# Kernel optimization log

Measured on AMD Instinct MI355X. Metric: run time of the kernel, lower is better.

Reference implementation:

```python
import jax, jax.numpy as jnp
import numpy as np

B, N, C = 256, 196, 256
RES, RES_, STRIDE = 14, 7, 2
H, KD, D = 16, 16, 64          # heads, key_dim, d=attn_ratio*key_dim
NH_KD, DH = H * KD, H * D      # 256, 1024
HW = DH + NH_KD                # kv width 1280
OUT = 512
EPS = 1e-5
SCALE = KD ** -0.5


def make_bias_idxs():
    pts = [(i, j) for i in range(RES) for j in range(RES)]
    pts_ = [(i, j) for i in range(RES_) for j in range(RES_)]
    offsets, idxs = {}, []
    for p1 in pts_:
        for p2 in pts:
            off = (abs(p1[0] * STRIDE - p2[0]), abs(p1[1] * STRIDE - p2[1]))
            if off not in offsets:
                offsets[off] = len(offsets)
            idxs.append(offsets[off])
    return np.array(idxs, np.int32).reshape(len(pts_), len(pts)), len(offsets)


def bn(x, g, b, m, v):
    return (x - m) * (g / jnp.sqrt(v + EPS)) + b


def hardswish(x):
    return x * jnp.clip(x + 3.0, 0.0, 6.0) / 6.0


def setup_inputs() -> dict:
    key = jax.random.key(0)
    ks = jax.random.split(key, 12)
    idxs, n_off = make_bias_idxs()
    s_in, s_dh = (2.0 / C) ** 0.5, (2.0 / DH) ** 0.5
    return {
        "x": jax.random.normal(ks[0], (B, N, C), jnp.float32),
        "W_kv": jax.random.normal(ks[1], (HW, C), jnp.float32) * s_in,
        "g_kv": jnp.ones((HW,)), "b_kv": jnp.zeros((HW,)),
        "m_kv": jax.random.normal(ks[2], (HW,)) * 0.1,
        "v_kv": jax.random.uniform(ks[3], (HW,), minval=0.5, maxval=1.5),
        "W_q": jax.random.normal(ks[4], (NH_KD, C), jnp.float32) * s_in,
        "g_q": jnp.ones((NH_KD,)), "b_q": jnp.zeros((NH_KD,)),
        "m_q": jax.random.normal(ks[5], (NH_KD,)) * 0.1,
        "v_q": jax.random.uniform(ks[6], (NH_KD,), minval=0.5, maxval=1.5),
        "W_p": jax.random.normal(ks[7], (OUT, DH), jnp.float32) * s_dh,
        "g_p": jnp.ones((OUT,)), "b_p": jnp.zeros((OUT,)),
        "m_p": jax.random.normal(ks[8], (OUT,)) * 0.1,
        "v_p": jax.random.uniform(ks[9], (OUT,), minval=0.5, maxval=1.5),
        "attn_biases": jax.random.normal(ks[10], (H, n_off), jnp.float32) * 0.02,
        "bias_idxs": jnp.asarray(idxs),
    }


def reference(x, W_kv, g_kv, b_kv, m_kv, v_kv, W_q, g_q, b_q, m_q, v_q,
              W_p, g_p, b_p, m_p, v_p, attn_biases, bias_idxs):
    # kv branch: Linear(no bias) + BN over flattened tokens
    kv = bn(jnp.einsum('bnc,hc->bnh', x, W_kv), g_kv, b_kv, m_kv, v_kv)
    kv = kv.reshape(B, N, H, KD + D)
    k, v = kv[..., :KD], kv[..., KD:]                 # [B,N,H,KD], [B,N,H,D]
    # q branch: spatial subsample stride 2 then LinearNorm
    xs = x.reshape(B, RES, RES, C)[:, ::STRIDE, ::STRIDE].reshape(B, RES_ * RES_, C)
    q = bn(jnp.einsum('bnc,hc->bnh', xs, W_q), g_q, b_q, m_q, v_q)
    q = q.reshape(B, RES_ * RES_, H, KD)              # [B,49,H,KD]
    bias = attn_biases[:, bias_idxs]                  # [H,49,196]
    attn = jnp.einsum('bqhd,bkhd->bhqk', q, k) * SCALE + bias
    attn = jax.nn.softmax(attn, axis=-1)
    o = jnp.einsum('bhqk,bkhd->bqhd', attn, v).reshape(B, RES_ * RES_, DH)
    return bn(jnp.einsum('bnd,od->bno', hardswish(o), W_p), g_p, b_p, m_p, v_p)
```

## Files before the change

kernel.cpp:

```cpp
#include <hip/hip_runtime.h>

typedef unsigned short u16;
typedef unsigned int u32;
typedef __attribute__((ext_vector_type(8))) short bf16x8;
typedef __attribute__((ext_vector_type(4))) float f32x4;

__device__ __forceinline__ u16 f2bf(float x) {
  union { float f; u32 u; } un; un.f = x;
  u32 r = un.u + 0x7FFFu + ((un.u >> 16) & 1u);
  return (u16)(r >> 16);
}

__device__ __forceinline__ void gl_lds16(const u16* gsrc, u16* ldst) {
  __builtin_amdgcn_global_load_lds(
      (const __attribute__((address_space(1))) void*)gsrc,
      (__attribute__((address_space(3))) void*)ldst,
      16, 0, 0);
}

__global__ __launch_bounds__(256) void prep_misc(
    const float* __restrict__ Wkv, const float* __restrict__ Wq, const float* __restrict__ Wp,
    const float* __restrict__ gkv, const float* __restrict__ bkv, const float* __restrict__ mkv, const float* __restrict__ vkv,
    const float* __restrict__ gq, const float* __restrict__ bq, const float* __restrict__ mq, const float* __restrict__ vq,
    const float* __restrict__ gp, const float* __restrict__ bp, const float* __restrict__ mp, const float* __restrict__ vp,
    const float* __restrict__ ab, const int* __restrict__ bidx,
    u16* __restrict__ wkvb, u16* __restrict__ wqb, u16* __restrict__ wpb,
    float* __restrict__ skv, float* __restrict__ tkv,
    float* __restrict__ sq, float* __restrict__ tq,
    float* __restrict__ sp, float* __restrict__ tp,
    float* __restrict__ biasf)
{
  int i = blockIdx.x * 256 + threadIdx.x;
  if (i < 327680) { wkvb[i] = f2bf(Wkv[i]); return; }
  i -= 327680;
  if (i < 65536) { wqb[i] = f2bf(Wq[i]); return; }
  i -= 65536;
  if (i < 524288) { wpb[i] = f2bf(Wp[i]); return; }
  i -= 524288;
  if (i < 153664) { biasf[i] = ab[(i / 9604) * 196 + bidx[i % 9604]]; return; }
  i -= 153664;
  if (i < 1280) { float s = gkv[i] * rsqrtf(vkv[i] + 1e-5f); skv[i] = s; tkv[i] = bkv[i] - mkv[i] * s; return; }
  i -= 1280;
  if (i < 256) {
    int h = i >> 4, c = i & 15;
    float sk = gkv[h * 80 + c] * rsqrtf(vkv[h * 80 + c] + 1e-5f);
    float s = gq[i] * rsqrtf(vq[i] + 1e-5f);
    sq[i] = s * 0.25f * sk;
    tq[i] = (bq[i] - mq[i] * s) * 0.25f * sk;
    return;
  }
  i -= 256;
  if (i < 512) { float s = gp[i] * rsqrtf(vp[i] + 1e-5f); sp[i] = s; tp[i] = bp[i] - mp[i] * s; return; }
}

__global__ __launch_bounds__(256) void conv_x(const float* __restrict__ x, u16* __restrict__ xb)
{
  int u = blockIdx.x * 256 + threadIdx.x;
  float4 v = ((const float4*)x)[u];
  uint2 o;
  o.x = (u32)f2bf(v.x) | ((u32)f2bf(v.y) << 16);
  o.y = (u32)f2bf(v.z) | ((u32)f2bf(v.w) << 16);
  ((uint2*)xb)[u] = o;
}

__global__ __launch_bounds__(256) void gemm_bn(
    const u16* __restrict__ A, const u16* __restrict__ W,
    const float* __restrict__ sv, const float* __restrict__ tv,
    float* __restrict__ outp, int N, int K, int NBLK)
{
  __shared__ u16 As[128 * 64];
  __shared__ u16 Bs[128 * 64];
  const int tid = threadIdx.x;
  const int lane = tid & 63;
  const int wv = tid >> 6, wr = wv >> 1, wc = wv & 1;
  const int lo = lane & 15, hi = lane >> 4;

  int bid = blockIdx.x;
  int cpx = gridDim.x >> 3;
  int wg = (bid & 7) * cpx + (bid >> 3);
  const int m0 = (wg / NBLK) * 128, n0 = (wg % NBLK) * 128;

  f32x4 zero4 = {0.f, 0.f, 0.f, 0.f};
  f32x4 acc[4][4];
#pragma unroll
  for (int m = 0; m < 4; ++m)
#pragma unroll
    for (int n = 0; n < 4; ++n) acc[m][n] = zero4;

  for (int kt = 0; kt < K; kt += 64) {
    __syncthreads();
#pragma unroll
    for (int i = 0; i < 4; ++i) {
      int e = (i * 256 + tid) * 8;
      int r = e >> 6, c = e & 63;
      int cs = c ^ ((r & 7) << 3);
      gl_lds16(A + (long)(m0 + r) * K + (kt + cs), As + e);
      gl_lds16(W + (long)(n0 + r) * K + (kt + cs), Bs + e);
    }
    __syncthreads();
#pragma unroll
    for (int kk = 0; kk < 64; kk += 32) {
      bf16x8 af[4], bfr[4];
#pragma unroll
      for (int m = 0; m < 4; ++m)
        af[m] = *(const bf16x8*)(As + (wr * 64 + m * 16 + lo) * 64 + ((kk + hi * 8) ^ ((lo & 7) << 3)));
#pragma unroll
      for (int n = 0; n < 4; ++n)
        bfr[n] = *(const bf16x8*)(Bs + (wc * 64 + n * 16 + lo) * 64 + ((kk + hi * 8) ^ ((lo & 7) << 3)));
#pragma unroll
      for (int m = 0; m < 4; ++m)
#pragma unroll
        for (int n = 0; n < 4; ++n)
          acc[m][n] = __builtin_amdgcn_mfma_f32_16x16x32_bf16(af[m], bfr[n], acc[m][n], 0, 0, 0);
    }
  }
#pragma unroll
  for (int m = 0; m < 4; ++m) {
    const int row0 = m0 + wr * 64 + m * 16 + hi * 4;
#pragma unroll
    for (int n = 0; n < 4; ++n) {
      const int col = n0 + wc * 64 + n * 16 + lo;
      const float s = sv[col], t = tv[col];
#pragma unroll
      for (int j = 0; j < 4; ++j)
        outp[(long)(row0 + j) * N + col] = acc[m][n][j] * s + t;
    }
  }
}

#define WOFF  13312
#define VTS   208
#define KOFF  13312
#define KS    24
#define QOFF  18304
#define QS    24
#define POFF  13312
#define PS    208
#define SMEM_N 26624

__device__ __forceinline__ int swz(int col, int rowkey) {
  return (col < 192) ? (col ^ ((rowkey & 7) << 3)) : col;
}

__global__ __launch_bounds__(256, 3) void fused_attn(
    const u16* __restrict__ xb, const u16* __restrict__ wkvb, const u16* __restrict__ wqb,
    const float* __restrict__ skv, const float* __restrict__ tkv,
    const float* __restrict__ sqv, const float* __restrict__ tqv,
    const float* __restrict__ biasf, u16* __restrict__ osw)
{
  __shared__ __align__(16) u16 sm[SMEM_N];
  const int tid = threadIdx.x;
  const int bid = blockIdx.x;
  const int wg = (bid & 7) * 512 + (bid >> 3);
  const int bb = wg >> 4, hh = wg & 15;
  const int w = tid >> 6, lane = tid & 63, lo = lane & 15, hi = lane >> 4;

  const u16* xbase = xb + (long)bb * 196 * 256;
  const u16* wkvh = wkvb + (long)hh * 80 * 256;
  const u16* wqh  = wqb + (long)hh * 16 * 256;

  f32x4 z4 = {0.f, 0.f, 0.f, 0.f};
  f32x4 acc[3][5];
#pragma unroll
  for (int u = 0; u < 3; ++u)
#pragma unroll
    for (int nf = 0; nf < 5; ++nf) acc[u][nf] = z4;
  f32x4 acc12a = z4, acc12b = z4;
  f32x4 qacc = z4;

  int qi = w * 16 + lo; if (qi > 48) qi = 48;
  const int gr = (qi / 7) * 28 + (qi % 7) * 2;

  for (int kt = 0; kt < 256; kt += 64) {
    __syncthreads();
#pragma unroll
    for (int i = 0; i < 7; ++i) {
      if (i < 6 || tid < 128) {
        int e = (i * 256 + tid) * 8;
        int r = e >> 6, c = e & 63;
        int xr = (r < 196) ? r : 195;
        int cs = c ^ ((r & 7) << 3);
        gl_lds16(xbase + (long)xr * 256 + kt + cs, sm + e);
      }
    }
#pragma unroll
    for (int i = 0; i < 3; ++i) {
      int e = (i * 256 + tid) * 8;
      int r = e >> 6, c = e & 63;
      int cs = c ^ ((r & 7) << 3);
      const u16* src = (r < 80) ? (wkvh + (long)r * 256 + kt + cs)
                                : (wqh + (long)(r - 80) * 256 + kt + cs);
      gl_lds16(src, sm + WOFF + e);
    }
    __syncthreads();
    __builtin_amdgcn_s_setprio(1);
#pragma unroll
    for (int kk = 0; kk < 64; kk += 32) {
      const int csw = (kk + hi * 8) ^ ((lo & 7) << 3);
      bf16x8 bfr[6];
#pragma unroll
      for (int nf = 0; nf < 6; ++nf)
        bfr[nf] = *(const bf16x8*)(sm + WOFF + (nf * 16 + lo) * 64 + csw);
      {
        bf16x8 aqf = *(const bf16x8*)(sm + gr * 64 + ((kk + hi * 8) ^ ((gr & 7) << 3)));
        qacc = __builtin_amdgcn_mfma_f32_16x16x32_bf16(aqf, bfr[5], qacc, 0, 0, 0);
      }
#pragma unroll
      for (int u = 0; u < 3; ++u) {
        const int mf = w + u * 4;
        bf16x8 af = *(const bf16x8*)(sm + (mf * 16 + lo) * 64 + csw);
#pragma unroll
        for (int nf = 0; nf < 5; ++nf)
          acc[u][nf] = __builtin_amdgcn_mfma_f32_16x16x32_bf16(af, bfr[nf], acc[u][nf], 0, 0, 0);
      }
      if (w) {
        bf16x8 af12 = *(const bf16x8*)(sm + (192 + lo) * 64 + csw);
        if (w == 1) {
          acc12a = __builtin_amdgcn_mfma_f32_16x16x32_bf16(af12, bfr[0], acc12a, 0, 0, 0);
          acc12b = __builtin_amdgcn_mfma_f32_16x16x32_bf16(af12, bfr[1], acc12b, 0, 0, 0);
        } else if (w == 2) {
          acc12a = __builtin_amdgcn_mfma_f32_16x16x32_bf16(af12, bfr[2], acc12a, 0, 0, 0);
          acc12b = __builtin_amdgcn_mfma_f32_16x16x32_bf16(af12, bfr[3], acc12b, 0, 0, 0);
        } else {
          acc12a = __builtin_amdgcn_mfma_f32_16x16x32_bf16(af12, bfr[4], acc12a, 0, 0, 0);
        }
      }
    }
    __builtin_amdgcn_s_setprio(0);
  }
  __syncthreads();

#pragma unroll
  for (int u = 0; u < 3; ++u) {
    const int mf = w + u * 4;
    const int nnb = mf * 16 + hi * 4;
#pragma unroll
    for (int j = 0; j < 4; ++j)
      sm[KOFF + (nnb + j) * KS + lo] = f2bf(acc[u][0][j]);
#pragma unroll
    for (int nf = 1; nf < 5; ++nf) {
      const int d = nf * 16 - 16 + lo;
      uint2 pp;
      pp.x = (u32)f2bf(acc[u][nf][0]) | ((u32)f2bf(acc[u][nf][1]) << 16);
      pp.y = (u32)f2bf(acc[u][nf][2]) | ((u32)f2bf(acc[u][nf][3]) << 16);
      *(uint2*)(sm + d * VTS + swz(nnb, d)) = pp;
    }
  }
  {
    const int nnb = 192 + hi * 4;
    if (w == 1) {
#pragma unroll
      for (int j = 0; j < 4; ++j)
        sm[KOFF + (nnb + j) * KS + lo] = f2bf(acc12a[j]);
      const int d = lo;
      uint2 pp;
      pp.x = (u32)f2bf(acc12b[0]) | ((u32)f2bf(acc12b[1]) << 16);
      pp.y = (u32)f2bf(acc12b[2]) | ((u32)f2bf(acc12b[3]) << 16);
      *(uint2*)(sm + d * VTS + swz(nnb, d)) = pp;
    } else if (w == 2) {
      const int d0 = 16 + lo, d1 = 32 + lo;
      uint2 pa, pb;
      pa.x = (u32)f2bf(acc12a[0]) | ((u32)f2bf(acc12a[1]) << 16);
      pa.y = (u32)f2bf(acc12a[2]) | ((u32)f2bf(acc12a[3]) << 16);
      pb.x = (u32)f2bf(acc12b[0]) | ((u32)f2bf(acc12b[1]) << 16);
      pb.y = (u32)f2bf(acc12b[2]) | ((u32)f2bf(acc12b[3]) << 16);
      *(uint2*)(sm + d0 * VTS + swz(nnb, d0)) = pa;
      *(uint2*)(sm + d1 * VTS + swz(nnb, d1)) = pb;
    } else if (w == 3) {
      const int d = 48 + lo;
      uint2 pp;
      pp.x = (u32)f2bf(acc12a[0]) | ((u32)f2bf(acc12a[1]) << 16);
      pp.y = (u32)f2bf(acc12a[2]) | ((u32)f2bf(acc12a[3]) << 16);
      *(uint2*)(sm + d * VTS + swz(nnb, d)) = pp;
    }
  }
  {
    const float s = sqv[hh * 16 + lo], t = tqv[hh * 16 + lo];
#pragma unroll
    for (int j = 0; j < 4; ++j) {
      const int r = w * 16 + hi * 4 + j;
      sm[QOFF + r * QS + lo] = f2bf(qacc[j] * s + t);
    }
  }
  __syncthreads();

  f32x4 sc[13];
  {
    bf16x8 zf = {0, 0, 0, 0, 0, 0, 0, 0};
    bf16x8 aq2 = zf;
    if (hi < 2) aq2 = *(const bf16x8*)(sm + QOFF + (w * 16 + lo) * QS + hi * 8);
#pragma unroll
    for (int t13 = 0; t13 < 13; ++t13) {
      bf16x8 bk = zf;
      if (hi < 2) bk = *(const bf16x8*)(sm + KOFF + (t13 * 16 + lo) * KS + hi * 8);
      sc[t13] = __builtin_amdgcn_mfma_f32_16x16x32_bf16(aq2, bk, z4, 0, 0, 0);
    }
  }
  __syncthreads();

  float rs[4];
#pragma unroll
  for (int j = 0; j < 4; ++j) {
    const int row = w * 16 + hi * 4 + j;
    const int rb = (row < 49) ? row : 0;
    float vals[13];
#pragma unroll
    for (int t = 0; t < 13; ++t) {
      const int col = t * 16 + lo;
      vals[t] = (col < 196) ? sc[t][j] + biasf[(hh * 49 + rb) * 196 + col] : -1e30f;
    }
    float mx = vals[0];
#pragma unroll
    for (int t = 1; t < 13; ++t) mx = fmaxf(mx, vals[t]);
#pragma unroll
    for (int s = 1; s < 16; s <<= 1) mx = fmaxf(mx, __shfl_xor(mx, s, 64));
    float sum = 0.f;
#pragma unroll
    for (int t = 0; t < 13; ++t) { float p = __expf(vals[t] - mx); vals[t] = p; sum += p; }
#pragma unroll
    for (int s = 1; s < 16; s <<= 1) sum += __shfl_xor(sum, s, 64);
#pragma unroll
    for (int t = 0; t < 13; ++t) sm[POFF + row * PS + swz(t * 16 + lo, row)] = f2bf(vals[t]);
    rs[j] = sum;
  }

  f32x4 oacc[4];
#pragma unroll
  for (int n = 0; n < 4; ++n) oacc[n] = z4;
  __builtin_amdgcn_s_setprio(1);
#pragma unroll
  for (int kt = 0; kt < 192; kt += 32) {
    bf16x8 ap = *(const bf16x8*)(sm + POFF + (w * 16 + lo) * PS + ((kt + hi * 8) ^ ((lo & 7) << 3)));
#pragma unroll
    for (int n = 0; n < 4; ++n) {
      bf16x8 bv = *(const bf16x8*)(sm + (n * 16 + lo) * VTS + ((kt + hi * 8) ^ ((lo & 7) << 3)));
      oacc[n] = __builtin_amdgcn_mfma_f32_16x16x32_bf16(ap, bv, oacc[n], 0, 0, 0);
    }
  }
  {
    bf16x8 zf = {0, 0, 0, 0, 0, 0, 0, 0};
    bf16x8 ap = zf;
    if (hi < 2) ap = *(const bf16x8*)(sm + POFF + (w * 16 + lo) * PS + 192 + hi * 8);
#pragma unroll
    for (int n = 0; n < 4; ++n) {
      bf16x8 bv = zf;
      if (hi < 2) bv = *(const bf16x8*)(sm + (n * 16 + lo) * VTS + 192 + hi * 8);
      oacc[n] = __builtin_amdgcn_mfma_f32_16x16x32_bf16(ap, bv, oacc[n], 0, 0, 0);
    }
  }
  __builtin_amdgcn_s_setprio(0);

  float svv[4], tvv[4];
#pragma unroll
  for (int n = 0; n < 4; ++n) {
    svv[n] = skv[hh * 80 + 16 + n * 16 + lo];
    tvv[n] = tkv[hh * 80 + 16 + n * 16 + lo];
  }
#pragma unroll
  for (int j = 0; j < 4; ++j) {
    const int row = w * 16 + hi * 4 + j;
    if (row < 49) {
      const float rinv = 1.f / rs[j];
      const long ob = ((long)(bb * 49 + row)) * 1024 + hh * 64 + lo;
#pragma unroll
      for (int n = 0; n < 4; ++n) {
        float val = oacc[n][j] * svv[n] * rinv + tvv[n];
        float hs = val * fminf(fmaxf(val + 3.f, 0.f), 6.f) * (1.f / 6.f);
        osw[ob + n * 16] = f2bf(hs);
      }
    }
  }
}

extern "C" void kernel_launch(void* const* d_in, const int* in_sizes, int n_in,
                              void* d_out, int out_size, void* d_ws, size_t ws_size,
                              hipStream_t stream)
{
  const float* x   = (const float*)d_in[0];
  const float* Wkv = (const float*)d_in[1];
  const float* gkv = (const float*)d_in[2];
  const float* bkv = (const float*)d_in[3];
  const float* mkv = (const float*)d_in[4];
  const float* vkv = (const float*)d_in[5];
  const float* Wq  = (const float*)d_in[6];
  const float* gq  = (const float*)d_in[7];
  const float* bq  = (const float*)d_in[8];
  const float* mq  = (const float*)d_in[9];
  const float* vq  = (const float*)d_in[10];
  const float* Wp  = (const float*)d_in[11];
  const float* gp  = (const float*)d_in[12];
  const float* bp  = (const float*)d_in[13];
  const float* mp  = (const float*)d_in[14];
  const float* vp  = (const float*)d_in[15];
  const float* ab  = (const float*)d_in[16];
  const int* bidx  = (const int*)d_in[17];

  char* ws = (char*)d_ws;
  size_t off = 0;
  auto alloc = [&](size_t bytes) -> char* {
    char* p = ws + off;
    off += (bytes + 255) & ~(size_t)255;
    return p;
  };
  u16* x_bf   = (u16*)alloc((size_t)50176 * 256 * 2);
  u16* wkv_bf = (u16*)alloc((size_t)1280 * 256 * 2);
  u16* wq_bf  = (u16*)alloc((size_t)256 * 256 * 2);
  u16* wp_bf  = (u16*)alloc((size_t)512 * 1024 * 2);
  u16* hsw    = (u16*)alloc((size_t)12544 * 1024 * 2);
  float* bias_f = (float*)alloc((size_t)153664 * 4);
  float* s_kv = (float*)alloc(1280 * 4);
  float* t_kv = (float*)alloc(1280 * 4);
  float* s_q  = (float*)alloc(256 * 4);
  float* t_q  = (float*)alloc(256 * 4);
  float* s_p  = (float*)alloc(512 * 4);
  float* t_p  = (float*)alloc(512 * 4);
  if (off > ws_size) return;

  prep_misc<<<4193, 256, 0, stream>>>(Wkv, Wq, Wp, gkv, bkv, mkv, vkv,
                                      gq, bq, mq, vq, gp, bp, mp, vp,
                                      ab, bidx, wkv_bf, wq_bf, wp_bf,
                                      s_kv, t_kv, s_q, t_q, s_p, t_p, bias_f);
  conv_x<<<12544, 256, 0, stream>>>(x, x_bf);
  fused_attn<<<4096, 256, 0, stream>>>(x_bf, wkv_bf, wq_bf, s_kv, t_kv, s_q, t_q, bias_f, hsw);
  gemm_bn<<<392, 256, 0, stream>>>(hsw, wp_bf, s_p, t_p, (float*)d_out, 512, 1024, 4);
}
```

Baseline: 125.7 us.

## Load x fragments directly from global and double-buffer weight tiles in LDS

The fused attention kernel no longer stages x tiles in LDS. Each wave reads its A fragments (kv rows, the tail rows and the strided q rows) straight from global memory as 16-byte vectors. The LDS tile of W_kv/W_q is now double-buffered, so the next K slice is prefetched while the current one is computed, with one barrier per iteration. This removes the LDS staging traffic and a barrier for x, but exposes global-load latency on the MFMA operand path and relies on cache hits. The x workspace is padded so reads past the last batch's rows stay in bounds.

```diff
diff --git a/kernel.cpp b/kernel.cpp
--- a/kernel.cpp
+++ b/kernel.cpp
@@ -128,7 +128,6 @@
   }
 }
 
-#define WOFF  13312
 #define VTS   208
 #define KOFF  13312
 #define KS    24
@@ -168,53 +167,64 @@
   f32x4 acc12a = z4, acc12b = z4;
   f32x4 qacc = z4;
 
+  const u16* rowA[3];
+#pragma unroll
+  for (int u = 0; u < 3; ++u) rowA[u] = xbase + (long)((w + u * 4) * 16 + lo) * 256;
+  int r12 = 192 + lo; if (r12 > 195) r12 = 195;
+  const u16* row12 = xbase + (long)r12 * 256;
   int qi = w * 16 + lo; if (qi > 48) qi = 48;
-  const int gr = (qi / 7) * 28 + (qi % 7) * 2;
-
-  for (int kt = 0; kt < 256; kt += 64) {
-    __syncthreads();
-#pragma unroll
-    for (int i = 0; i < 7; ++i) {
-      if (i < 6 || tid < 128) {
+  const u16* rowQ = xbase + (long)((qi / 7) * 28 + (qi % 7) * 2) * 256;
+
+#pragma unroll
+  for (int i = 0; i < 3; ++i) {
+    int e = (i * 256 + tid) * 8;
+    int r = e >> 6, c = e & 63;
+    int cs = c ^ ((r & 7) << 3);
+    const u16* src = (r < 80) ? (wkvh + (long)r * 256 + cs)
+                              : (wqh + (long)(r - 80) * 256 + cs);
+    gl_lds16(src, sm + e);
+  }
+  __syncthreads();
+
+#pragma unroll
+  for (int t = 0; t < 4; ++t) {
+    const int kt = t * 64;
+    const int WB = (t & 1) * 6144;
+    if (t < 3) {
+      const int kt2 = kt + 64;
+      const int WN = ((t + 1) & 1) * 6144;
+#pragma unroll
+      for (int i = 0; i < 3; ++i) {
         int e = (i * 256 + tid) * 8;
         int r = e >> 6, c = e & 63;
-        int xr = (r < 196) ? r : 195;
         int cs = c ^ ((r & 7) << 3);
-        gl_lds16(xbase + (long)xr * 256 + kt + cs, sm + e);
+        const u16* src = (r < 80) ? (wkvh + (long)r * 256 + kt2 + cs)
+                                  : (wqh + (long)(r - 80) * 256 + kt2 + cs);
+        gl_lds16(src, sm + WN + e);
       }
     }
-#pragma unroll
-    for (int i = 0; i < 3; ++i) {
-      int e = (i * 256 + tid) * 8;
-      int r = e >> 6, c = e & 63;
-      int cs = c ^ ((r & 7) << 3);
-      const u16* src = (r < 80) ? (wkvh + (long)r * 256 + kt + cs)
-                                : (wqh + (long)(r - 80) * 256 + kt + cs);
-      gl_lds16(src, sm + WOFF + e);
-    }
-    __syncthreads();
     __builtin_amdgcn_s_setprio(1);
 #pragma unroll
     for (int kk = 0; kk < 64; kk += 32) {
       const int csw = (kk + hi * 8) ^ ((lo & 7) << 3);
+      const int kg = kt + kk + hi * 8;
       bf16x8 bfr[6];
 #pragma unroll
       for (int nf = 0; nf < 6; ++nf)
-        bfr[nf] = *(const bf16x8*)(sm + WOFF + (nf * 16 + lo) * 64 + csw);
+        bfr[nf] = *(const bf16x8*)(sm + WB + (nf * 16 + lo) * 64 + csw);
       {
-        bf16x8 aqf = *(const bf16x8*)(sm + gr * 64 + ((kk + hi * 8) ^ ((gr & 7) << 3)));
+        bf16x8 aqf = *(const bf16x8*)(rowQ + kg);
         qacc = __builtin_amdgcn_mfma_f32_16x16x32_bf16(aqf, bfr[5], qacc, 0, 0, 0);
       }
 #pragma unroll
       for (int u = 0; u < 3; ++u) {
-        const int mf = w + u * 4;
-        bf16x8 af = *(const bf16x8*)(sm + (mf * 16 + lo) * 64 + csw);
+        bf16x8 af = *(const bf16x8*)(rowA[u] + kg);
 #pragma unroll
         for (int nf = 0; nf < 5; ++nf)
           acc[u][nf] = __builtin_amdgcn_mfma_f32_16x16x32_bf16(af, bfr[nf], acc[u][nf], 0, 0, 0);
       }
       if (w) {
-        bf16x8 af12 = *(const bf16x8*)(sm + (192 + lo) * 64 + csw);
+        bf16x8 af12 = *(const bf16x8*)(row12 + kg);
         if (w == 1) {
           acc12a = __builtin_amdgcn_mfma_f32_16x16x32_bf16(af12, bfr[0], acc12a, 0, 0, 0);
           acc12b = __builtin_amdgcn_mfma_f32_16x16x32_bf16(af12, bfr[1], acc12b, 0, 0, 0);
@@ -227,8 +237,8 @@
       }
     }
     __builtin_amdgcn_s_setprio(0);
-  }
-  __syncthreads();
+    __syncthreads();
+  }
 
 #pragma unroll
   for (int u = 0; u < 3; ++u) {
@@ -402,7 +412,7 @@
     off += (bytes + 255) & ~(size_t)255;
     return p;
   };
-  u16* x_bf   = (u16*)alloc((size_t)50176 * 256 * 2);
+  u16* x_bf   = (u16*)alloc((size_t)50176 * 256 * 2 + 8192);
   u16* wkv_bf = (u16*)alloc((size_t)1280 * 256 * 2);
   u16* wq_bf  = (u16*)alloc((size_t)256 * 256 * 2);
   u16* wp_bf  = (u16*)alloc((size_t)512 * 1024 * 2);
```

Result: slower. 168.5 us (+34.1%).

## Double-buffer the KV/Q projection K-loop with 32-wide stages

Applied to the files above, without the earlier changes.

Replaces the single-buffered 64-wide K tile loop in fused_attn with a double-buffered pipeline of 32-wide stages. The next stage's global-to-LDS loads are issued before computing the current one, and there is one barrier per step instead of two. The swizzle pattern is changed to suit the narrower rows. This aims to hide global load latency behind MFMA work, at the cost of more loop iterations and barriers, and it keeps the same LDS footprint.

```diff
diff --git a/kernel.cpp b/kernel.cpp
--- a/kernel.cpp
+++ b/kernel.cpp
@@ -128,7 +128,6 @@
   }
 }
 
-#define WOFF  13312
 #define VTS   208
 #define KOFF  13312
 #define KS    24
@@ -171,50 +170,65 @@
   int qi = w * 16 + lo; if (qi > 48) qi = 48;
   const int gr = (qi / 7) * 28 + (qi % 7) * 2;
 
-  for (int kt = 0; kt < 256; kt += 64) {
-    __syncthreads();
-#pragma unroll
-    for (int i = 0; i < 7; ++i) {
-      if (i < 6 || tid < 128) {
-        int e = (i * 256 + tid) * 8;
-        int r = e >> 6, c = e & 63;
+  const int kx = ((lo >> 1) & 3) << 3;
+  const int kq = ((gr >> 1) & 3) << 3;
+
+  auto stage = [&](int t) {
+    const int kt = t * 32;
+    u16* xbuf = sm + (t & 1) * 6656;
+    u16* wbuf = sm + 13312 + (t & 1) * 3072;
+#pragma unroll
+    for (int i = 0; i < 4; ++i) {
+      int idx = i * 256 + tid;
+      if (idx < 832) {
+        int e = idx * 8;
+        int r = e >> 5, c = e & 31;
         int xr = (r < 196) ? r : 195;
-        int cs = c ^ ((r & 7) << 3);
-        gl_lds16(xbase + (long)xr * 256 + kt + cs, sm + e);
-      }
-    }
-#pragma unroll
-    for (int i = 0; i < 3; ++i) {
-      int e = (i * 256 + tid) * 8;
-      int r = e >> 6, c = e & 63;
-      int cs = c ^ ((r & 7) << 3);
-      const u16* src = (r < 80) ? (wkvh + (long)r * 256 + kt + cs)
-                                : (wqh + (long)(r - 80) * 256 + kt + cs);
-      gl_lds16(src, sm + WOFF + e);
-    }
-    __syncthreads();
+        int cs = c ^ (((r >> 1) & 3) << 3);
+        gl_lds16(xbase + (long)xr * 256 + kt + cs, xbuf + e);
+      }
+    }
+#pragma unroll
+    for (int i = 0; i < 2; ++i) {
+      int idx = i * 256 + tid;
+      if (idx < 384) {
+        int e = idx * 8;
+        int r = e >> 5, c = e & 31;
+        int cs = c ^ (((r >> 1) & 3) << 3);
+        const u16* src = (r < 80) ? (wkvh + (long)r * 256 + kt + cs)
+                                  : (wqh + (long)(r - 80) * 256 + kt + cs);
+        gl_lds16(src, wbuf + e);
+      }
+    }
+  };
+
+  stage(0);
+  __syncthreads();
+#pragma unroll
+  for (int t = 0; t < 8; ++t) {
+    if (t < 7) stage(t + 1);
+    const u16* xbuf = sm + (t & 1) * 6656;
+    const u16* wbuf = sm + 13312 + (t & 1) * 3072;
+    const int ra = hi * 8;
     __builtin_amdgcn_s_setprio(1);
-#pragma unroll
-    for (int kk = 0; kk < 64; kk += 32) {
-      const int csw = (kk + hi * 8) ^ ((lo & 7) << 3);
+    {
       bf16x8 bfr[6];
 #pragma unroll
       for (int nf = 0; nf < 6; ++nf)
-        bfr[nf] = *(const bf16x8*)(sm + WOFF + (nf * 16 + lo) * 64 + csw);
+        bfr[nf] = *(const bf16x8*)(wbuf + (nf * 16 + lo) * 32 + (ra ^ kx));
       {
-        bf16x8 aqf = *(const bf16x8*)(sm + gr * 64 + ((kk + hi * 8) ^ ((gr & 7) << 3)));
+        bf16x8 aqf = *(const bf16x8*)(xbuf + gr * 32 + (ra ^ kq));
         qacc = __builtin_amdgcn_mfma_f32_16x16x32_bf16(aqf, bfr[5], qacc, 0, 0, 0);
       }
 #pragma unroll
       for (int u = 0; u < 3; ++u) {
-        const int mf = w + u * 4;
-        bf16x8 af = *(const bf16x8*)(sm + (mf * 16 + lo) * 64 + csw);
+        bf16x8 af = *(const bf16x8*)(xbuf + ((w + u * 4) * 16 + lo) * 32 + (ra ^ kx));
 #pragma unroll
         for (int nf = 0; nf < 5; ++nf)
           acc[u][nf] = __builtin_amdgcn_mfma_f32_16x16x32_bf16(af, bfr[nf], acc[u][nf], 0, 0, 0);
       }
       if (w) {
-        bf16x8 af12 = *(const bf16x8*)(sm + (192 + lo) * 64 + csw);
+        bf16x8 af12 = *(const bf16x8*)(xbuf + (192 + lo) * 32 + (ra ^ kx));
         if (w == 1) {
           acc12a = __builtin_amdgcn_mfma_f32_16x16x32_bf16(af12, bfr[0], acc12a, 0, 0, 0);
           acc12b = __builtin_amdgcn_mfma_f32_16x16x32_bf16(af12, bfr[1], acc12b, 0, 0, 0);
@@ -227,8 +241,8 @@
       }
     }
     __builtin_amdgcn_s_setprio(0);
-  }
-  __syncthreads();
+    __syncthreads();
+  }
 
 #pragma unroll
   for (int u = 0; u < 3; ++u) {
```

Result: no change. 125.8 us (+0.1%).

## Split softmax P staging into two LDS halves to shrink shared memory

Applied to the files above, without the earlier changes.

The probability matrix P is now written to LDS in two halves (columns 0-111, then 112-207) through a smaller 112-wide buffer with a new swizzle. The second half is kept in the score registers until the first PV pass finishes. This cuts the LDS footprint from 26624 to 20480 halfwords and raises launch bounds to 4 blocks per CU for more occupancy. The cost is extra register pressure from holding the scores, one more PV loop and a second LDS write phase. Each wave reads back only its own P rows, which is presumably why no extra barrier was added between the phases.

```diff
diff --git a/kernel.cpp b/kernel.cpp
--- a/kernel.cpp
+++ b/kernel.cpp
@@ -9,6 +9,9 @@
   union { float f; u32 u; } un; un.f = x;
   u32 r = un.u + 0x7FFFu + ((un.u >> 16) & 1u);
   return (u16)(r >> 16);
+}
+__device__ __forceinline__ u32 pk2(float a, float b) {
+  return (u32)f2bf(a) | ((u32)f2bf(b) << 16);
 }
 
 __device__ __forceinline__ void gl_lds16(const u16* gsrc, u16* ldst) {
@@ -128,21 +131,23 @@
   }
 }
 
-#define WOFF  13312
 #define VTS   208
 #define KOFF  13312
 #define KS    24
 #define QOFF  18304
 #define QS    24
-#define POFF  13312
-#define PS    208
-#define SMEM_N 26624
+#define PHOFF 13312
+#define PHS   112
+#define SMEM_N 20480
 
 __device__ __forceinline__ int swz(int col, int rowkey) {
   return (col < 192) ? (col ^ ((rowkey & 7) << 3)) : col;
 }
-
-__global__ __launch_bounds__(256, 3) void fused_attn(
+__device__ __forceinline__ int pswz(int col, int row) {
+  return (col < 96) ? (col ^ (((row >> 2) & 3) << 3)) : col;
+}
+
+__global__ __launch_bounds__(256, 4) void fused_attn(
     const u16* __restrict__ xb, const u16* __restrict__ wkvb, const u16* __restrict__ wqb,
     const float* __restrict__ skv, const float* __restrict__ tkv,
     const float* __restrict__ sqv, const float* __restrict__ tqv,
@@ -190,7 +195,7 @@
       int cs = c ^ ((r & 7) << 3);
       const u16* src = (r < 80) ? (wkvh + (long)r * 256 + kt + cs)
                                 : (wqh + (long)(r - 80) * 256 + kt + cs);
-      gl_lds16(src, sm + WOFF + e);
+      gl_lds16(src, sm + 13312 + e);
     }
     __syncthreads();
     __builtin_amdgcn_s_setprio(1);
@@ -200,7 +205,7 @@
       bf16x8 bfr[6];
 #pragma unroll
       for (int nf = 0; nf < 6; ++nf)
-        bfr[nf] = *(const bf16x8*)(sm + WOFF + (nf * 16 + lo) * 64 + csw);
+        bfr[nf] = *(const bf16x8*)(sm + 13312 + (nf * 16 + lo) * 64 + csw);
       {
         bf16x8 aqf = *(const bf16x8*)(sm + gr * 64 + ((kk + hi * 8) ^ ((gr & 7) << 3)));
         qacc = __builtin_amdgcn_mfma_f32_16x16x32_bf16(aqf, bfr[5], qacc, 0, 0, 0);
@@ -241,8 +246,8 @@
     for (int nf = 1; nf < 5; ++nf) {
       const int d = nf * 16 - 16 + lo;
       uint2 pp;
-      pp.x = (u32)f2bf(acc[u][nf][0]) | ((u32)f2bf(acc[u][nf][1]) << 16);
-      pp.y = (u32)f2bf(acc[u][nf][2]) | ((u32)f2bf(acc[u][nf][3]) << 16);
+      pp.x = pk2(acc[u][nf][0], acc[u][nf][1]);
+      pp.y = pk2(acc[u][nf][2], acc[u][nf][3]);
       *(uint2*)(sm + d * VTS + swz(nnb, d)) = pp;
     }
   }
@@ -254,23 +259,23 @@
         sm[KOFF + (nnb + j) * KS + lo] = f2bf(acc12a[j]);
       const int d = lo;
       uint2 pp;
-      pp.x = (u32)f2bf(acc12b[0]) | ((u32)f2bf(acc12b[1]) << 16);
-      pp.y = (u32)f2bf(acc12b[2]) | ((u32)f2bf(acc12b[3]) << 16);
+      pp.x = pk2(acc12b[0], acc12b[1]);
+      pp.y = pk2(acc12b[2], acc12b[3]);
       *(uint2*)(sm + d * VTS + swz(nnb, d)) = pp;
     } else if (w == 2) {
       const int d0 = 16 + lo, d1 = 32 + lo;
       uint2 pa, pb;
-      pa.x = (u32)f2bf(acc12a[0]) | ((u32)f2bf(acc12a[1]) << 16);
-      pa.y = (u32)f2bf(acc12a[2]) | ((u32)f2bf(acc12a[3]) << 16);
-      pb.x = (u32)f2bf(acc12b[0]) | ((u32)f2bf(acc12b[1]) << 16);
-      pb.y = (u32)f2bf(acc12b[2]) | ((u32)f2bf(acc12b[3]) << 16);
+      pa.x = pk2(acc12a[0], acc12a[1]);
+      pa.y = pk2(acc12a[2], acc12a[3]);
+      pb.x = pk2(acc12b[0], acc12b[1]);
+      pb.y = pk2(acc12b[2], acc12b[3]);
       *(uint2*)(sm + d0 * VTS + swz(nnb, d0)) = pa;
       *(uint2*)(sm + d1 * VTS + swz(nnb, d1)) = pb;
     } else if (w == 3) {
       const int d = 48 + lo;
       uint2 pp;
-      pp.x = (u32)f2bf(acc12a[0]) | ((u32)f2bf(acc12a[1]) << 16);
-      pp.y = (u32)f2bf(acc12a[2]) | ((u32)f2bf(acc12a[3]) << 16);
+      pp.x = pk2(acc12a[0], acc12a[1]);
+      pp.y = pk2(acc12a[2], acc12a[3]);
       *(uint2*)(sm + d * VTS + swz(nnb, d)) = pp;
     }
   }
@@ -320,17 +325,22 @@
 #pragma unroll
     for (int s = 1; s < 16; s <<= 1) sum += __shfl_xor(sum, s, 64);
 #pragma unroll
-    for (int t = 0; t < 13; ++t) sm[POFF + row * PS + swz(t * 16 + lo, row)] = f2bf(vals[t]);
+    for (int t = 0; t < 7; ++t)
+      sm[PHOFF + row * PHS + pswz(t * 16 + lo, row)] = f2bf(vals[t]);
+#pragma unroll
+    for (int t = 7; t < 13; ++t) sc[t][j] = vals[t];
     rs[j] = sum;
   }
 
   f32x4 oacc[4];
 #pragma unroll
   for (int n = 0; n < 4; ++n) oacc[n] = z4;
+  const int prow = w * 16 + lo;
+  const int pkey = ((lo >> 2) & 3) << 3;
   __builtin_amdgcn_s_setprio(1);
 #pragma unroll
-  for (int kt = 0; kt < 192; kt += 32) {
-    bf16x8 ap = *(const bf16x8*)(sm + POFF + (w * 16 + lo) * PS + ((kt + hi * 8) ^ ((lo & 7) << 3)));
+  for (int kt = 0; kt < 96; kt += 32) {
+    bf16x8 ap = *(const bf16x8*)(sm + PHOFF + prow * PHS + ((kt + hi * 8) ^ pkey));
 #pragma unroll
     for (int n = 0; n < 4; ++n) {
       bf16x8 bv = *(const bf16x8*)(sm + (n * 16 + lo) * VTS + ((kt + hi * 8) ^ ((lo & 7) << 3)));
@@ -340,11 +350,30 @@
   {
     bf16x8 zf = {0, 0, 0, 0, 0, 0, 0, 0};
     bf16x8 ap = zf;
-    if (hi < 2) ap = *(const bf16x8*)(sm + POFF + (w * 16 + lo) * PS + 192 + hi * 8);
+    if (hi < 2) ap = *(const bf16x8*)(sm + PHOFF + prow * PHS + 96 + hi * 8);
 #pragma unroll
     for (int n = 0; n < 4; ++n) {
       bf16x8 bv = zf;
-      if (hi < 2) bv = *(const bf16x8*)(sm + (n * 16 + lo) * VTS + 192 + hi * 8);
+      if (hi < 2) bv = *(const bf16x8*)(sm + (n * 16 + lo) * VTS + ((96 + hi * 8) ^ ((lo & 7) << 3)));
+      oacc[n] = __builtin_amdgcn_mfma_f32_16x16x32_bf16(ap, bv, oacc[n], 0, 0, 0);
+    }
+  }
+
+#pragma unroll
+  for (int j = 0; j < 4; ++j) {
+    const int row = w * 16 + hi * 4 + j;
+#pragma unroll
+    for (int t = 7; t < 13; ++t)
+      sm[PHOFF + row * PHS + pswz((t - 7) * 16 + lo, row)] = f2bf(sc[t][j]);
+  }
+
+#pragma unroll
+  for (int kl = 0; kl < 96; kl += 32) {
+    bf16x8 ap = *(const bf16x8*)(sm + PHOFF + prow * PHS + ((kl + hi * 8) ^ pkey));
+#pragma unroll
+    for (int n = 0; n < 4; ++n) {
+      const int lc = 112 + kl + hi * 8;
+      bf16x8 bv = *(const bf16x8*)(sm + (n * 16 + lo) * VTS + swz(lc, lo));
       oacc[n] = __builtin_amdgcn_mfma_f32_16x16x32_bf16(ap, bv, oacc[n], 0, 0, 0);
     }
   }
```

New measurement: 136.6 us. +8.7%, slower.
